# Kernel tuning notes

Hardware: AMD Instinct MI355X
Metric: run time of the kernel (lower is better)

## Reference

```python
import jax, jax.numpy as jnp
from jax import lax
import numpy as np

B, IN, J, S, F, O, C, KS = 8, 8, 8, 187, 64, 64, 67, 15


def _ln(x, eps=1e-5):
    m = jnp.mean(x, axis=-1, keepdims=True)
    v = jnp.mean((x - m) ** 2, axis=-1, keepdims=True)
    return (x - m) / jnp.sqrt(v + eps)


def setup_inputs() -> dict:
    key = jax.random.key(0)
    ks = jax.random.split(key, 8)
    x_in = jax.random.normal(ks[0], (B, IN, S, F), jnp.float32)
    proj_x_prev = jax.random.normal(ks[1], (B, IN, S, O), jnp.float32)
    lin = jnp.linspace(-1.0, 1.0, C, dtype=jnp.float32)
    spline_weights = jnp.broadcast_to(lin, (IN, J, C)) + 0.01 * jax.random.normal(ks[2], (IN, J, C), jnp.float32)
    tau = 0.1 * jax.random.normal(ks[3], (IN, J), jnp.float32) + 0.1
    temperature = jnp.asarray(1.0, jnp.float32)
    omiga = jnp.full((IN, J), 0.2, jnp.float32)
    W2 = jax.random.normal(ks[4], (J, F, O), jnp.float32) * (1.0 / np.sqrt(F))
    b_param = 0.02 * jax.random.normal(ks[5], (J, S, O), jnp.float32)
    ln_scale = jnp.ones((J, F), jnp.float32)
    ln_bias = jnp.zeros((J, F), jnp.float32)
    alpha = jnp.ones((J,), jnp.float32)
    beta = jnp.ones((J,), jnp.float32)
    theta = jnp.ones((J,), jnp.float32)
    gamma = jnp.ones((J,), jnp.float32)
    w3 = 0.1 * jax.random.normal(ks[6], (J, O, KS), jnp.float32)  # depthwise conv kernels
    return dict(x_in=x_in, proj_x_prev=proj_x_prev, spline_weights=spline_weights, tau=tau,
                temperature=temperature, omiga=omiga, W2=W2, b_param=b_param, ln_scale=ln_scale,
                ln_bias=ln_bias, alpha=alpha, beta=beta, theta=theta, gamma=gamma, w3=w3)


def reference(x_in, proj_x_prev, spline_weights, tau, temperature, omiga, W2, b_param,
              ln_scale, ln_bias, alpha, beta, theta, gamma, w3):
    b, in_n, seq, feat = x_in.shape
    out_n, nC = spline_weights.shape[1], spline_weights.shape[2]
    kk = w3.shape[-1]
    # --- cubic B-spline basis ---
    h = 2.0 / (nC - 1)
    grid = jnp.linspace(-1.0, 1.0, nC, dtype=x_in.dtype)
    max_val = jnp.max(jnp.abs(x_in)) + 1e-8
    xn = jnp.clip(x_in / max_val * 0.95, -0.99, 0.99)
    dist = jnp.abs(xn[..., None] - grid) / h  # [b,in,seq,feat,C]
    basis = jax.nn.relu(2.0 - dist) ** 3 / 6.0 - jax.nn.relu(1.0 - dist) ** 3 * (4.0 / 6.0)
    spline_mapping = jnp.einsum('bisfc,ijc->bijsf', basis, spline_weights)
    activated = spline_mapping + jnp.abs(omiga)[None, :, :, None, None] * x_in[:, :, None]
    # --- energy-threshold gating ---
    energies = jnp.mean(activated ** 2, axis=(-1, -2))  # [b,in,out]
    tau_a = jnp.abs(tau)[None]
    t_val = jnp.abs(temperature) * np.sqrt(seq / 256.0) + 1e-4
    sqrtE = jnp.sqrt(energies + 1e-8)
    mask = jax.nn.sigmoid((sqrtE - tau_a) / t_val)  # [b,in,out]
    mult = sqrtE / (tau_a + 1e-8)
    wp = proj_x_prev[:, :, None] * (mult * mask)[..., None, None]  # [b,in,out,seq,d]
    d = wp.shape[-1]
    mid = in_n // 2
    Kt = wp[:, 0::2].transpose(0, 2, 3, 1, 4).reshape(b, out_n, seq, mid * d)
    Qt = wp[:, 1::2].transpose(0, 2, 3, 1, 4).reshape(b, out_n, seq, mid * d)
    Kt, Qt = _ln(Kt), _ln(Qt)
    raw = jnp.einsum('bjse,bjte->bjst', Kt, Qt)
    W1 = jax.nn.softmax(raw / (np.sqrt(mid * d) * t_val), axis=-1)  # [b,out,seq,seq]
    combined = jnp.einsum('bijsf,bij->bjsf', activated, mask)  # [b,out,seq,feat]
    # --- SplineWeightLayer (vectorized over out_n) ---
    xln = _ln(combined) * ln_scale[None, :, None, :] + ln_bias[None, :, None, :]
    x_prime = jnp.einsum('bjsh,jho->bjso', xln, W2) + b_param[None]  # [b,out,seq,O]
    o = x_prime.shape[-1]
    xt = x_prime.transpose(0, 2, 1, 3).reshape(b, seq, out_n * o)
    ker = w3.transpose(2, 0, 1).reshape(kk, 1, out_n * o)
    w3f = lax.conv_general_dilated(xt, ker, (1,), [(kk // 2, kk // 2)],
                                   dimension_numbers=('NWC', 'WIO', 'NWC'),
                                   feature_group_count=out_n * o)
    w3f = w3f.reshape(b, seq, out_n, o).transpose(0, 2, 1, 3)
    eye = jnp.eye(seq, dtype=x_in.dtype)
    attn_kernel = jnp.abs(beta)[None, :, None, None] * W1 + jnp.abs(alpha)[None, :, None, None] * eye
    global_part = jnp.einsum('bjst,bjto->bjso', attn_kernel, x_prime)
    spatial = global_part + jnp.abs(theta)[None, :, None, None] * w3f
    out = spatial + gamma[None, :, None, None] * combined  # residual_proj is Identity (F==O)
    return out, x_prime
```

## Files before the change

kernel.cpp:

```cpp
#include <hip/hip_runtime.h>
#include <math.h>

#define B_N 8
#define IN_N 8
#define J_N 8
#define S_N 187
#define F_N 64
#define O_N 64
#define C_N 67
#define KS_N 15
#define SF_N (S_N * F_N)
#define SF4_N (SF_N / 4)
#define SQRT_SF 0.85467470f

#define NT_SPL 12
#define NCOMB 384
#define NKT16 768
#define NXPR 768
#define NRF 768
#define NMAXP 256
#define FRAG_BJ 49152

typedef __attribute__((ext_vector_type(8))) _Float16 half8;
typedef __attribute__((ext_vector_type(4))) _Float16 half4;
typedef __attribute__((ext_vector_type(4))) float floatx4;

__device__ __forceinline__ float wave_sum(float v) {
#pragma unroll
  for (int off = 32; off > 0; off >>= 1) v += __shfl_down(v, off, 64);
  return __shfl(v, 0, 64);
}
__device__ __forceinline__ float wave_max(float v) {
#pragma unroll
  for (int off = 32; off > 0; off >>= 1) v = fmaxf(v, __shfl_down(v, off, 64));
  return __shfl(v, 0, 64);
}
__device__ __forceinline__ float lane_bc(float v, int l) {
  return __int_as_float(__builtin_amdgcn_readlane(__float_as_int(v), l));
}
__device__ __forceinline__ float bspline(float d) {
  float t2 = fmaxf(2.f - d, 0.f);
  float t1 = fmaxf(1.f - d, 0.f);
  return t2 * t2 * t2 * (1.f / 6.f) - t1 * t1 * t1 * (4.f / 6.f);
}
__device__ __forceinline__ float get_inv095(const float* __restrict__ maxp) {
  int lane = threadIdx.x & 63;
  float m = 0.f;
#pragma unroll
  for (int k = 0; k < NMAXP / 64; k++) m = fmaxf(m, maxp[lane + k * 64]);
  return 0.95f / (wave_max(m) + 1e-8f);
}
__device__ __forceinline__ float gate_g(const float* __restrict__ esum_p, int bi, int j,
                                        const float* __restrict__ tau, float tv) {
  const float* p = esum_p + ((long)bi * 8 + j) * NT_SPL;
  float s = 0.f;
#pragma unroll
  for (int k = 0; k < NT_SPL; k++) s += p[k];
  float sE = sqrtf(s * (1.f / (float)SF_N) + 1e-8f);
  float ta = fabsf(tau[(bi & 7) * 8 + j]);
  return (sE / (ta + 1e-8f)) / (1.f + expf(-(sE - ta) / tv));
}

__global__ void k_maxabs(const float4* __restrict__ x, float* __restrict__ maxp, int n4) {
  __shared__ float red[4];
  int tid = blockIdx.x * 256 + threadIdx.x;
  float m = 0.f;
  for (int i = tid; i < n4; i += gridDim.x * 256) {
    float4 v = x[i];
    m = fmaxf(m, fmaxf(fmaxf(fabsf(v.x), fabsf(v.y)), fmaxf(fabsf(v.z), fabsf(v.w))));
  }
  m = wave_max(m);
  if ((threadIdx.x & 63) == 0) red[threadIdx.x >> 6] = m;
  __syncthreads();
  if (threadIdx.x == 0)
    maxp[blockIdx.x] = fmaxf(fmaxf(red[0], red[1]), fmaxf(red[2], red[3]));
}

__global__ void k_spline(const float4* __restrict__ x4, const float* __restrict__ sw,
                         const float* __restrict__ omiga, const float* __restrict__ maxp,
                         float4* __restrict__ act4, float* __restrict__ esum_p) {
  int tile = blockIdx.x, bi = blockIdx.y;
  int i = bi & 7;
  __shared__ float wl[J_N * C_N];
  __shared__ float aom[J_N];
  __shared__ float red[4 * J_N];
  for (int t = threadIdx.x; t < J_N * C_N; t += 256) wl[t] = sw[i * J_N * C_N + t];
  if (threadIdx.x < J_N) aom[threadIdx.x] = fabsf(omiga[i * J_N + threadIdx.x]);
  int lane = threadIdx.x & 63, wid = threadIdx.x >> 6;
  float inv = get_inv095(maxp);
  __syncthreads();
  int i4 = tile * 256 + threadIdx.x;
  float e[J_N] = {0, 0, 0, 0, 0, 0, 0, 0};
  if (i4 < SF4_N) {
    float4 xv = x4[(long)bi * SF4_N + i4];
    float xs[4] = {xv.x, xv.y, xv.z, xv.w};
    float4 av[J_N];
#pragma unroll
    for (int c = 0; c < 4; c++) {
      float x = xs[c];
      float xn = fminf(fmaxf(x * inv, -0.99f), 0.99f);
      float u = (xn + 1.f) * 33.f;
      int c0 = (int)floorf(u) - 1;
      float sm[J_N] = {0, 0, 0, 0, 0, 0, 0, 0};
#pragma unroll
      for (int kk = 0; kk < 4; kk++) {
        int cc = c0 + kk;
        if (cc >= 0 && cc < C_N) {
          float bas = bspline(fabsf(u - (float)cc));
#pragma unroll
          for (int j = 0; j < J_N; j++) sm[j] += bas * wl[j * C_N + cc];
        }
      }
#pragma unroll
      for (int j = 0; j < J_N; j++) {
        float a = sm[j] + aom[j] * x;
        (&av[j].x)[c] = a;
        e[j] += a * a;
      }
    }
#pragma unroll
    for (int j = 0; j < J_N; j++) act4[((long)(bi * 8 + j)) * SF4_N + i4] = av[j];
  }
#pragma unroll
  for (int j = 0; j < J_N; j++) {
    float v = e[j];
#pragma unroll
    for (int off = 32; off > 0; off >>= 1) v += __shfl_down(v, off, 64);
    if (lane == 0) red[wid * J_N + j] = v;
  }
  __syncthreads();
  if (threadIdx.x < J_N)
    esum_p[((long)bi * 8 + threadIdx.x) * NT_SPL + tile] =
        red[threadIdx.x] + red[8 + threadIdx.x] + red[16 + threadIdx.x] + red[24 + threadIdx.x];
}

__global__ void k_mid2(const float4* __restrict__ act4, const float* __restrict__ esum_p,
                       const float* __restrict__ tau, const float* __restrict__ temp,
                       const float* __restrict__ proj, float4* __restrict__ comb4,
                       _Float16* __restrict__ khi, _Float16* __restrict__ klo,
                       _Float16* __restrict__ qhi, _Float16* __restrict__ qlo) {
  __shared__ _Float16 stg[4][4096];
  __shared__ float mk[16];
  int lane = threadIdx.x & 63;
  if (blockIdx.x < NCOMB) {
    int blk = blockIdx.x;
    int tile = blk % 12, bjg = blk / 12;
    int jg = bjg & 3, b = bjg >> 2;
    int j0 = jg * 2;
    if (threadIdx.x < 16) {
      int i = threadIdx.x >> 1, j = j0 + (threadIdx.x & 1);
      const float* p = esum_p + ((long)(b * 8 + i) * 8 + j) * NT_SPL;
      float s = 0.f;
#pragma unroll
      for (int k = 0; k < NT_SPL; k++) s += p[k];
      float sE = sqrtf(s * (1.f / (float)SF_N) + 1e-8f);
      float ta = fabsf(tau[i * 8 + j]);
      float tv = fabsf(temp[0]) * SQRT_SF + 1e-4f;
      mk[threadIdx.x] = 1.f / (1.f + expf(-(sE - ta) / tv));
    }
    __syncthreads();
    int i4 = tile * 256 + threadIdx.x;
    if (i4 < SF4_N) {
      float4 cb[2] = {};
#pragma unroll
      for (int i = 0; i < IN_N; i++) {
#pragma unroll
        for (int jj = 0; jj < 2; jj++) {
          float4 a = act4[((long)((b * 8 + i) * 8 + j0 + jj)) * SF4_N + i4];
          float g = mk[i * 2 + jj];
          cb[jj].x += g * a.x; cb[jj].y += g * a.y;
          cb[jj].z += g * a.z; cb[jj].w += g * a.w;
        }
      }
#pragma unroll
      for (int jj = 0; jj < 2; jj++)
        comb4[((long)(b * J_N + j0 + jj)) * SF4_N + i4] = cb[jj];
    }
  } else {
    int blk = blockIdx.x - NCOMB;
    int bj = blk / 12, stile = blk - bj * 12;
    int b = bj >> 3, j = bj & 7;
    int w = threadIdx.x >> 6;
    int ig = lane >> 4;
    int f4 = (lane & 15) * 4;
    int iK = b * 8 + 2 * ig, iQ = iK + 1;
    float tv = fabsf(temp[0]) * SQRT_SF + 1e-4f;
    float gK = gate_g(esum_p, iK, j, tau, tv);
    float gQ = gate_g(esum_p, iQ, j, tau, tv);
    int slotbase = (lane >> 3) * 512 + ((lane >> 1) & 3) * 128 + (lane & 1) * 4;
    for (int rr = 0; rr < 4; rr++) {
      int m16 = w * 4 + rr;
      int s = stile * 16 + m16;
      half4 hk4 = {}, lk4 = {}, hq4 = {}, lq4 = {};
      if (s < S_N) {
        float4 kr = *(const float4*)(proj + ((long)iK * S_N + s) * 64 + f4);
        float4 qr = *(const float4*)(proj + ((long)iQ * S_N + s) * 64 + f4);
        float kv[4] = {kr.x * gK, kr.y * gK, kr.z * gK, kr.w * gK};
        float qv[4] = {qr.x * gQ, qr.y * gQ, qr.z * gQ, qr.w * gQ};
        float mkv = wave_sum(kv[0] + kv[1] + kv[2] + kv[3]) * (1.f / 256.f);
        float mqv = wave_sum(qv[0] + qv[1] + qv[2] + qv[3]) * (1.f / 256.f);
        float vk = 0.f, vq = 0.f;
#pragma unroll
        for (int q = 0; q < 4; q++) {
          float dk = kv[q] - mkv; vk += dk * dk;
          float dq = qv[q] - mqv; vq += dq * dq;
        }
        vk = wave_sum(vk) * (1.f / 256.f);
        vq = wave_sum(vq) * (1.f / 256.f);
        float ik = 1.f / sqrtf(vk + 1e-5f);
        float iq = 1.f / sqrtf(vq + 1e-5f);
#pragma unroll
        for (int q = 0; q < 4; q++) {
          float fk = (kv[q] - mkv) * ik;
          float fq = (qv[q] - mqv) * iq;
          _Float16 hk = (_Float16)fk;
          _Float16 hq = (_Float16)fq;
          hk4[q] = hk; lk4[q] = (_Float16)(fk - (float)hk);
          hq4[q] = hq; lq4[q] = (_Float16)(fq - (float)hq);
        }
      }
      int off = slotbase + m16 * 8;
      *(half4*)&stg[0][off] = hk4;
      *(half4*)&stg[1][off] = lk4;
      *(half4*)&stg[2][off] = hq4;
      *(half4*)&stg[3][off] = lq4;
    }
    __syncthreads();
    long gb = ((long)bj * 12 + stile) * 4096;
    float4* dk = (float4*)(khi + gb);
    float4* dkl = (float4*)(klo + gb);
    float4* dq = (float4*)(qhi + gb);
    float4* dql = (float4*)(qlo + gb);
    const float4* s0 = (const float4*)stg[0];
    const float4* s1 = (const float4*)stg[1];
    const float4* s2 = (const float4*)stg[2];
    const float4* s3 = (const float4*)stg[3];
    int t = threadIdx.x;
    dk[t] = s0[t];  dk[t + 256] = s0[t + 256];
    dkl[t] = s1[t]; dkl[t + 256] = s1[t + 256];
    dq[t] = s2[t];  dq[t + 256] = s2[t + 256];
    dql[t] = s3[t]; dql[t + 256] = s3[t + 256];
  }
}

__global__ void k_xp(const float* __restrict__ comb, const float* __restrict__ W2,
                     const float* __restrict__ bparam, const float* __restrict__ lns,
                     const float* __restrict__ lnb, float* __restrict__ xprime) {
  __shared__ float smem[64 * 64 + 128];
  int lane = threadIdx.x & 63;
  int tile = blockIdx.x % 12, bj = blockIdx.x / 12;
  int j = bj & 7;
  float* w2s = smem;
  float* lss = smem + 4096;
  float* lbs = smem + 4160;
  const float4* wg = (const float4*)(W2 + j * 4096);
  float4* ws4 = (float4*)w2s;
  for (int idx = threadIdx.x; idx < 1024; idx += 256) ws4[idx] = wg[idx];
  if (threadIdx.x < 64) {
    lss[threadIdx.x] = lns[j * 64 + threadIdx.x];
    lbs[threadIdx.x] = lnb[j * 64 + threadIdx.x];
  }
  __syncthreads();
  int w = threadIdx.x >> 6;
  int sbase = tile * 16 + w * 4;
  float xln[4], acc[4];
#pragma unroll
  for (int rr = 0; rr < 4; rr++) {
    int s = sbase + rr;
    int sc = (s < S_N) ? s : S_N - 1;
    float x = comb[((long)bj * S_N + sc) * 64 + lane];
    float m = wave_sum(x) * (1.f / 64.f);
    float d = x - m;
    float var = wave_sum(d * d) * (1.f / 64.f);
    xln[rr] = d / sqrtf(var + 1e-5f) * lss[lane] + lbs[lane];
    acc[rr] = bparam[(j * S_N + sc) * 64 + lane];
  }
#pragma unroll
  for (int h = 0; h < 64; h++) {
    float w2v = w2s[h * 64 + lane];
#pragma unroll
    for (int rr = 0; rr < 4; rr++) acc[rr] += lane_bc(xln[rr], h) * w2v;
  }
#pragma unroll
  for (int rr = 0; rr < 4; rr++) {
    int s = sbase + rr;
    if (s < S_N) xprime[((long)bj * S_N + s) * 64 + lane] = acc[rr];
  }
}

__global__ void k_rawfinal(const _Float16* __restrict__ khi, const _Float16* __restrict__ klo,
                           const _Float16* __restrict__ qhi, const _Float16* __restrict__ qlo,
                           const float* __restrict__ temp, const float* __restrict__ xprime,
                           const float* __restrict__ comb, const float* __restrict__ w3,
                           const float* __restrict__ alpha, const float* __restrict__ beta,
                           const float* __restrict__ theta, const float* __restrict__ gamma,
                           float* __restrict__ out) {
  __shared__ float w1t[16 * 188];
  int xcd = blockIdx.x & 7;
  int idx = blockIdx.x >> 3;
  int bj = xcd * 8 + idx / 12;
  int stile = idx - (idx / 12) * 12;
  int j = bj & 7;
  int w = threadIdx.x >> 6, lane = threadIdx.x & 63;
  int quad = lane >> 4, m16 = lane & 15;
  long fb = (long)bj * FRAG_BJ + lane * 8;
  const _Float16* ah_p = khi + fb + (long)stile * 4096;
  const _Float16* al_p = klo + fb + (long)stile * 4096;
  floatx4 acc[3] = {};
  for (int ec = 0; ec < 8; ec++) {
    half8 ah = *(const half8*)(ah_p + ec * 512);
    half8 al = *(const half8*)(al_p + ec * 512);
#pragma unroll
    for (int n = 0; n < 3; n++) {
      long bo = fb + (long)(w * 3 + n) * 4096 + ec * 512;
      half8 bh = *(const half8*)(qhi + bo);
      half8 bl = *(const half8*)(qlo + bo);
      acc[n] = __builtin_amdgcn_mfma_f32_16x16x32_f16(ah, bh, acc[n], 0, 0, 0);
      acc[n] = __builtin_amdgcn_mfma_f32_16x16x32_f16(al, bh, acc[n], 0, 0, 0);
      acc[n] = __builtin_amdgcn_mfma_f32_16x16x32_f16(ah, bl, acc[n], 0, 0, 0);
    }
  }
  float tv = fabsf(temp[0]) * SQRT_SF + 1e-4f;
  float scale = 1.f / (16.f * tv);
#pragma unroll
  for (int n = 0; n < 3; n++) {
    int t = (w * 3 + n) * 16 + m16;
    if (t < S_N) {
#pragma unroll
      for (int r = 0; r < 4; r++)
        w1t[(quad * 4 + r) * 188 + t] = acc[n][r] * scale;
    }
  }
  __syncthreads();
  int o = lane;
#pragma unroll
  for (int rr = 0; rr < 4; rr++) {
    float* row = &w1t[(w * 4 + rr) * 188];
    float v[3];
    float m = -1e30f;
#pragma unroll
    for (int q = 0; q < 3; q++) {
      int t = o + q * 64;
      v[q] = (t < S_N) ? row[t] : -1e30f;
      m = fmaxf(m, v[q]);
    }
    m = wave_max(m);
    float ssum = 0.f;
#pragma unroll
    for (int q = 0; q < 3; q++) {
      int t = o + q * 64;
      float e = (t < S_N) ? expf(v[q] - m) : 0.f;
      v[q] = e;
      ssum += e;
    }
    ssum = wave_sum(ssum);
    float invs = 1.f / ssum;
#pragma unroll
    for (int q = 0; q < 3; q++) {
      int t = o + q * 64;
      if (t < S_N) row[t] = v[q] * invs;
    }
  }
  __syncthreads();
  float w3c[KS_N];
#pragma unroll
  for (int k = 0; k < KS_N; k++) w3c[k] = w3[j * 64 * KS_N + o * KS_N + k];
  const float* xpg = xprime + (long)bj * (S_N * 64);
  float aa = fabsf(alpha[j]), ba = fabsf(beta[j]), ta = fabsf(theta[j]), gv = gamma[j];
  int s0 = stile * 16;
  float acc2[4] = {0.f, 0.f, 0.f, 0.f};
  for (int t = 0; t < 184; t += 4) {
    float x0 = xpg[t * 64 + o];
    float x1 = xpg[(t + 1) * 64 + o];
    float x2 = xpg[(t + 2) * 64 + o];
    float x3 = xpg[(t + 3) * 64 + o];
#pragma unroll
    for (int rr = 0; rr < 4; rr++) {
      float4 wv = *(const float4*)&w1t[(w * 4 + rr) * 188 + t];
      acc2[rr] += wv.x * x0 + wv.y * x1 + wv.z * x2 + wv.w * x3;
    }
  }
#pragma unroll
  for (int t = 184; t < S_N; t++) {
    float xv = xpg[t * 64 + o];
#pragma unroll
    for (int rr = 0; rr < 4; rr++) acc2[rr] += w1t[(w * 4 + rr) * 188 + t] * xv;
  }
#pragma unroll
  for (int rr = 0; rr < 4; rr++) {
    int s = s0 + w * 4 + rr;
    if (s >= S_N) continue;
    float conv = 0.f;
#pragma unroll
    for (int k = 0; k < KS_N; k++) {
      int si = s + k - 7;
      if (si >= 0 && si < S_N) conv += xpg[si * 64 + o] * w3c[k];
    }
    float res = ba * acc2[rr] + aa * xpg[s * 64 + o] + ta * conv +
                gv * comb[((long)bj * S_N + s) * 64 + o];
    out[((long)bj * S_N + s) * 64 + o] = res;
  }
}

extern "C" void kernel_launch(void* const* d_in, const int* in_sizes, int n_in,
                              void* d_out, int out_size, void* d_ws, size_t ws_size,
                              hipStream_t stream) {
  const float* x_in   = (const float*)d_in[0];
  const float* proj   = (const float*)d_in[1];
  const float* sw     = (const float*)d_in[2];
  const float* tau    = (const float*)d_in[3];
  const float* temp   = (const float*)d_in[4];
  const float* omiga  = (const float*)d_in[5];
  const float* W2     = (const float*)d_in[6];
  const float* bparam = (const float*)d_in[7];
  const float* lns    = (const float*)d_in[8];
  const float* lnb    = (const float*)d_in[9];
  const float* alpha  = (const float*)d_in[10];
  const float* beta   = (const float*)d_in[11];
  const float* theta  = (const float*)d_in[12];
  const float* gamma  = (const float*)d_in[13];
  const float* w3     = (const float*)d_in[14];

  float* out = (float*)d_out;
  float* xprime = out + B_N * J_N * S_N * O_N;

  float* wsf = (float*)d_ws;
  float* maxp   = wsf;
  float* esum_p = wsf + 512;
  float* act    = wsf + 512 + 512 * NT_SPL;
  const long ACT_N = (long)64 * 8 * SF_N;
  const long FR = (long)64 * FRAG_BJ;
  _Float16* khi = (_Float16*)(act + ACT_N);
  _Float16* klo = khi + FR;
  _Float16* qhi = klo + FR;
  _Float16* qlo = qhi + FR;
  float* comb = (float*)(qlo + FR);

  k_maxabs<<<NMAXP, 256, 0, stream>>>((const float4*)x_in, maxp, (B_N * IN_N * S_N * F_N) / 4);
  k_spline<<<dim3(NT_SPL, 64), 256, 0, stream>>>((const float4*)x_in, sw, omiga, maxp,
                                                 (float4*)act, esum_p);
  k_mid2<<<NCOMB + NKT16, 256, 0, stream>>>((const float4*)act, esum_p, tau, temp,
                                            proj, (float4*)comb, khi, klo, qhi, qlo);
  k_xp<<<NXPR, 256, 0, stream>>>(comb, W2, bparam, lns, lnb, xprime);
  k_rawfinal<<<NRF, 256, 0, stream>>>(khi, klo, qhi, qlo, temp, xprime, comb,
                                      w3, alpha, beta, theta, gamma, out);
}
```

Baseline: 161.8 us.

## Fuse LayerNorm+W2 projection into combine kernel and transpose spline weight layout

The separate k_xp kernel is removed. Its LayerNorm and W2 projection now run inside the combine branch of k_mid2, working on register-resident combined values through 16-lane shuffles, and W2 for two output channels is staged in shared memory. This saves a kernel launch and the global re-read of the combined tensor. In exchange, k_mid2 needs 33KB+ of shared memory, which can lower occupancy for both branches. Separately, the spline weights are transposed to a [C][8] layout so each basis term reads two float4s instead of eight scalar LDS loads.

```diff
diff --git a/kernel.cpp b/kernel.cpp
--- a/kernel.cpp
+++ b/kernel.cpp
@@ -16,7 +16,6 @@
 #define NT_SPL 12
 #define NCOMB 384
 #define NKT16 768
-#define NXPR 768
 #define NRF 768
 #define NMAXP 256
 #define FRAG_BJ 49152
@@ -34,9 +33,6 @@
 #pragma unroll
   for (int off = 32; off > 0; off >>= 1) v = fmaxf(v, __shfl_down(v, off, 64));
   return __shfl(v, 0, 64);
-}
-__device__ __forceinline__ float lane_bc(float v, int l) {
-  return __int_as_float(__builtin_amdgcn_readlane(__float_as_int(v), l));
 }
 __device__ __forceinline__ float bspline(float d) {
   float t2 = fmaxf(2.f - d, 0.f);
@@ -81,10 +77,13 @@
                          float4* __restrict__ act4, float* __restrict__ esum_p) {
   int tile = blockIdx.x, bi = blockIdx.y;
   int i = bi & 7;
-  __shared__ float wl[J_N * C_N];
+  __shared__ float wl[C_N * 8];
   __shared__ float aom[J_N];
   __shared__ float red[4 * J_N];
-  for (int t = threadIdx.x; t < J_N * C_N; t += 256) wl[t] = sw[i * J_N * C_N + t];
+  for (int t = threadIdx.x; t < J_N * C_N; t += 256) {
+    int j = t / C_N, c = t - j * C_N;
+    wl[c * 8 + j] = sw[i * J_N * C_N + t];
+  }
   if (threadIdx.x < J_N) aom[threadIdx.x] = fabsf(omiga[i * J_N + threadIdx.x]);
   int lane = threadIdx.x & 63, wid = threadIdx.x >> 6;
   float inv = get_inv095(maxp);
@@ -107,8 +106,12 @@
         int cc = c0 + kk;
         if (cc >= 0 && cc < C_N) {
           float bas = bspline(fabsf(u - (float)cc));
-#pragma unroll
-          for (int j = 0; j < J_N; j++) sm[j] += bas * wl[j * C_N + cc];
+          const float4* wp = (const float4*)(wl + cc * 8);
+          float4 wa = wp[0], wb = wp[1];
+          sm[0] += bas * wa.x; sm[1] += bas * wa.y;
+          sm[2] += bas * wa.z; sm[3] += bas * wa.w;
+          sm[4] += bas * wb.x; sm[5] += bas * wb.y;
+          sm[6] += bas * wb.z; sm[7] += bas * wb.w;
         }
       }
 #pragma unroll
@@ -136,17 +139,33 @@
 
 __global__ void k_mid2(const float4* __restrict__ act4, const float* __restrict__ esum_p,
                        const float* __restrict__ tau, const float* __restrict__ temp,
-                       const float* __restrict__ proj, float4* __restrict__ comb4,
+                       const float* __restrict__ proj, const float* __restrict__ W2,
+                       const float* __restrict__ bparam, const float* __restrict__ lns,
+                       const float* __restrict__ lnb, float4* __restrict__ comb4,
+                       float* __restrict__ xprime,
                        _Float16* __restrict__ khi, _Float16* __restrict__ klo,
                        _Float16* __restrict__ qhi, _Float16* __restrict__ qlo) {
-  __shared__ _Float16 stg[4][4096];
-  __shared__ float mk[16];
+  __shared__ float smem[8192 + 16 + 256];
   int lane = threadIdx.x & 63;
   if (blockIdx.x < NCOMB) {
     int blk = blockIdx.x;
     int tile = blk % 12, bjg = blk / 12;
     int jg = bjg & 3, b = bjg >> 2;
     int j0 = jg * 2;
+    float* w2s = smem;
+    float* mk  = smem + 8192;
+    float* lss = smem + 8208;
+    float* lbs = smem + 8336;
+    {
+      const float4* wg = (const float4*)(W2 + j0 * 4096);
+      float4* ws4 = (float4*)w2s;
+      for (int t = threadIdx.x; t < 2048; t += 256) ws4[t] = wg[t];
+    }
+    if (threadIdx.x < 128) {
+      int jj = threadIdx.x >> 6, f = threadIdx.x & 63;
+      lss[threadIdx.x] = lns[(j0 + jj) * 64 + f];
+      lbs[threadIdx.x] = lnb[(j0 + jj) * 64 + f];
+    }
     if (threadIdx.x < 16) {
       int i = threadIdx.x >> 1, j = j0 + (threadIdx.x & 1);
       const float* p = esum_p + ((long)(b * 8 + i) * 8 + j) * NT_SPL;
@@ -175,8 +194,50 @@
 #pragma unroll
       for (int jj = 0; jj < 2; jj++)
         comb4[((long)(b * J_N + j0 + jj)) * SF4_N + i4] = cb[jj];
+      int s = i4 >> 4;
+      int fx = (threadIdx.x & 15) * 4;
+      int g0 = lane & 48;
+#pragma unroll
+      for (int jj = 0; jj < 2; jj++) {
+        float4 c = cb[jj];
+        float ls = c.x + c.y + c.z + c.w;
+#pragma unroll
+        for (int m = 1; m <= 8; m <<= 1) ls += __shfl_xor(ls, m, 64);
+        float mean = ls * (1.f / 64.f);
+        float d0 = c.x - mean, d1 = c.y - mean, d2 = c.z - mean, d3 = c.w - mean;
+        float lv = d0 * d0 + d1 * d1 + d2 * d2 + d3 * d3;
+#pragma unroll
+        for (int m = 1; m <= 8; m <<= 1) lv += __shfl_xor(lv, m, 64);
+        float invsd = 1.f / sqrtf(lv * (1.f / 64.f) + 1e-5f);
+        float xln0 = d0 * invsd * lss[jj * 64 + fx + 0] + lbs[jj * 64 + fx + 0];
+        float xln1 = d1 * invsd * lss[jj * 64 + fx + 1] + lbs[jj * 64 + fx + 1];
+        float xln2 = d2 * invsd * lss[jj * 64 + fx + 2] + lbs[jj * 64 + fx + 2];
+        float xln3 = d3 * invsd * lss[jj * 64 + fx + 3] + lbs[jj * 64 + fx + 3];
+        float4 bp = *(const float4*)(bparam + ((long)(j0 + jj) * S_N + s) * 64 + fx);
+        float a0 = bp.x, a1 = bp.y, a2 = bp.z, a3 = bp.w;
+#pragma unroll
+        for (int t16 = 0; t16 < 16; t16++) {
+          int src = g0 + t16;
+          float h0 = __shfl(xln0, src, 64);
+          float h1 = __shfl(xln1, src, 64);
+          float h2 = __shfl(xln2, src, 64);
+          float h3 = __shfl(xln3, src, 64);
+          const float* wrow = w2s + jj * 4096 + (t16 * 4) * 64 + fx;
+          float4 w0 = *(const float4*)(wrow);
+          float4 w1 = *(const float4*)(wrow + 64);
+          float4 w2v = *(const float4*)(wrow + 128);
+          float4 w3v = *(const float4*)(wrow + 192);
+          a0 += h0 * w0.x + h1 * w1.x + h2 * w2v.x + h3 * w3v.x;
+          a1 += h0 * w0.y + h1 * w1.y + h2 * w2v.y + h3 * w3v.y;
+          a2 += h0 * w0.z + h1 * w1.z + h2 * w2v.z + h3 * w3v.z;
+          a3 += h0 * w0.w + h1 * w1.w + h2 * w2v.w + h3 * w3v.w;
+        }
+        float4 o4 = {a0, a1, a2, a3};
+        *(float4*)(xprime + (((long)(b * J_N + j0 + jj)) * S_N + s) * 64 + fx) = o4;
+      }
     }
   } else {
+    _Float16* stg = (_Float16*)smem;
     int blk = blockIdx.x - NCOMB;
     int bj = blk / 12, stile = blk - bj * 12;
     int b = bj >> 3, j = bj & 7;
@@ -220,10 +281,10 @@
         }
       }
       int off = slotbase + m16 * 8;
-      *(half4*)&stg[0][off] = hk4;
-      *(half4*)&stg[1][off] = lk4;
-      *(half4*)&stg[2][off] = hq4;
-      *(half4*)&stg[3][off] = lq4;
+      *(half4*)&stg[0 * 4096 + off] = hk4;
+      *(half4*)&stg[1 * 4096 + off] = lk4;
+      *(half4*)&stg[2 * 4096 + off] = hq4;
+      *(half4*)&stg[3 * 4096 + off] = lq4;
     }
     __syncthreads();
     long gb = ((long)bj * 12 + stile) * 4096;
@@ -231,60 +292,15 @@
     float4* dkl = (float4*)(klo + gb);
     float4* dq = (float4*)(qhi + gb);
     float4* dql = (float4*)(qlo + gb);
-    const float4* s0 = (const float4*)stg[0];
-    const float4* s1 = (const float4*)stg[1];
-    const float4* s2 = (const float4*)stg[2];
-    const float4* s3 = (const float4*)stg[3];
+    const float4* s0 = (const float4*)(stg + 0 * 4096);
+    const float4* s1 = (const float4*)(stg + 1 * 4096);
+    const float4* s2 = (const float4*)(stg + 2 * 4096);
+    const float4* s3 = (const float4*)(stg + 3 * 4096);
     int t = threadIdx.x;
     dk[t] = s0[t];  dk[t + 256] = s0[t + 256];
     dkl[t] = s1[t]; dkl[t + 256] = s1[t + 256];
     dq[t] = s2[t];  dq[t + 256] = s2[t + 256];
     dql[t] = s3[t]; dql[t + 256] = s3[t + 256];
-  }
-}
-
-__global__ void k_xp(const float* __restrict__ comb, const float* __restrict__ W2,
-                     const float* __restrict__ bparam, const float* __restrict__ lns,
-                     const float* __restrict__ lnb, float* __restrict__ xprime) {
-  __shared__ float smem[64 * 64 + 128];
-  int lane = threadIdx.x & 63;
-  int tile = blockIdx.x % 12, bj = blockIdx.x / 12;
-  int j = bj & 7;
-  float* w2s = smem;
-  float* lss = smem + 4096;
-  float* lbs = smem + 4160;
-  const float4* wg = (const float4*)(W2 + j * 4096);
-  float4* ws4 = (float4*)w2s;
-  for (int idx = threadIdx.x; idx < 1024; idx += 256) ws4[idx] = wg[idx];
-  if (threadIdx.x < 64) {
-    lss[threadIdx.x] = lns[j * 64 + threadIdx.x];
-    lbs[threadIdx.x] = lnb[j * 64 + threadIdx.x];
-  }
-  __syncthreads();
-  int w = threadIdx.x >> 6;
-  int sbase = tile * 16 + w * 4;
-  float xln[4], acc[4];
-#pragma unroll
-  for (int rr = 0; rr < 4; rr++) {
-    int s = sbase + rr;
-    int sc = (s < S_N) ? s : S_N - 1;
-    float x = comb[((long)bj * S_N + sc) * 64 + lane];
-    float m = wave_sum(x) * (1.f / 64.f);
-    float d = x - m;
-    float var = wave_sum(d * d) * (1.f / 64.f);
-    xln[rr] = d / sqrtf(var + 1e-5f) * lss[lane] + lbs[lane];
-    acc[rr] = bparam[(j * S_N + sc) * 64 + lane];
-  }
-#pragma unroll
-  for (int h = 0; h < 64; h++) {
-    float w2v = w2s[h * 64 + lane];
-#pragma unroll
-    for (int rr = 0; rr < 4; rr++) acc[rr] += lane_bc(xln[rr], h) * w2v;
-  }
-#pragma unroll
-  for (int rr = 0; rr < 4; rr++) {
-    int s = sbase + rr;
-    if (s < S_N) xprime[((long)bj * S_N + s) * 64 + lane] = acc[rr];
   }
 }
 
@@ -439,9 +455,9 @@
   k_maxabs<<<NMAXP, 256, 0, stream>>>((const float4*)x_in, maxp, (B_N * IN_N * S_N * F_N) / 4);
   k_spline<<<dim3(NT_SPL, 64), 256, 0, stream>>>((const float4*)x_in, sw, omiga, maxp,
                                                  (float4*)act, esum_p);
-  k_mid2<<<NCOMB + NKT16, 256, 0, stream>>>((const float4*)act, esum_p, tau, temp,
-                                            proj, (float4*)comb, khi, klo, qhi, qlo);
-  k_xp<<<NXPR, 256, 0, stream>>>(comb, W2, bparam, lns, lnb, xprime);
+  k_mid2<<<NCOMB + NKT16, 256, 0, stream>>>((const float4*)act, esum_p, tau, temp, proj,
+                                            W2, bparam, lns, lnb, (float4*)comb, xprime,
+                                            khi, klo, qhi, qlo);
   k_rawfinal<<<NRF, 256, 0, stream>>>(khi, klo, qhi, qlo, temp, xprime, comb,
                                       w3, alpha, beta, theta, gamma, out);
 }
```

After: 154.8 us. 1.05x faster.
